# Kernel tuning notes

Hardware: AMD Instinct MI355X
Metric: run time of the kernel (lower is better)

Reference implementation:

```python
import jax, jax.numpy as jnp
import numpy as np

N_NODES = 50000


def sage_conv(x, src, dst, Wl, bl, Wr):
    # PyG SAGEConv (aggr='mean'): out_i = Wl @ mean_{j in N(i)} x_j + bl + Wr @ x_i
    msg = x[src]                                              # [E, d] gather
    agg = jax.ops.segment_sum(msg, dst, num_segments=N_NODES)  # [N, d]
    cnt = jax.ops.segment_sum(jnp.ones((src.shape[0],), x.dtype), dst,
                              num_segments=N_NODES)
    mean = agg / jnp.maximum(cnt, 1.0)[:, None]
    return mean @ Wl.T + bl + x @ Wr.T


def graph_forward(x, edge_index, W1l, b1, W1r, W2l, b2, W2r):
    src, dst = edge_index[0], edge_index[1]
    h = jnp.tanh(sage_conv(x, src, dst, W1l, b1, W1r))
    return jnp.tanh(sage_conv(h, src, dst, W2l, b2, W2r))


def setup_inputs() -> dict:
    key = jax.random.key(0)
    ks = jax.random.split(key, 16)
    E = 800000
    IN, HID, OUT = 128, 256, 128
    s = lambda fan: 1.0 / np.sqrt(fan)
    inp = {
        'x0': jax.random.normal(ks[0], (N_NODES, IN), jnp.float32),
        'x1': jax.random.normal(ks[1], (N_NODES, IN), jnp.float32),
        'edge_index0': jax.random.randint(ks[2], (2, E), 0, N_NODES),
        'edge_index1': jax.random.randint(ks[3], (2, E), 0, N_NODES),
    }
    for g, base in ((0, 4), (1, 10)):
        inp[f'W1l_{g}'] = jax.random.normal(ks[base + 0], (HID, IN), jnp.float32) * s(IN)
        inp[f'b1_{g}'] = jnp.zeros((HID,), jnp.float32)
        inp[f'W1r_{g}'] = jax.random.normal(ks[base + 1], (HID, IN), jnp.float32) * s(IN)
        inp[f'W2l_{g}'] = jax.random.normal(ks[base + 2], (OUT, HID), jnp.float32) * s(HID)
        inp[f'b2_{g}'] = jnp.zeros((OUT,), jnp.float32)
        inp[f'W2r_{g}'] = jax.random.normal(ks[base + 3], (OUT, HID), jnp.float32) * s(HID)
    return inp


def reference(x0, x1, edge_index0, edge_index1,
              W1l_0, b1_0, W1r_0, W2l_0, b2_0, W2r_0,
              W1l_1, b1_1, W1r_1, W2l_1, b2_1, W2r_1):
    out0 = graph_forward(x0, edge_index0, W1l_0, b1_0, W1r_0, W2l_0, b2_0, W2r_0)
    out1 = graph_forward(x1, edge_index1, W1l_1, b1_1, W1r_1, W2l_1, b2_1, W2r_1)
    return jnp.concatenate([out0, out1], axis=0)
```

## Files before the change

### kernel.cpp

```cpp
#include <hip/hip_runtime.h>
#include <cstddef>

#define N_NODES 50000
#define N_EDGES 800000
#define CAP 64
#define XU (N_NODES * 16)
#define XRNG ((N_NODES + 7) / 8)

typedef __attribute__((ext_vector_type(8))) _Float16 half8;
typedef __attribute__((ext_vector_type(2))) _Float16 half2v;
typedef __attribute__((ext_vector_type(4))) float f32x4;
typedef __attribute__((ext_vector_type(4))) float f4v;
typedef __attribute__((ext_vector_type(2))) float f2v;

__device__ __forceinline__ float fast_tanh(float x) {
    float t = __expf(2.0f * x);
    return 1.0f - 2.0f / (t + 1.0f);
}

__global__ __launch_bounds__(256) void prep_k(
        const int* __restrict__ src0, const int* __restrict__ dst0,
        const int* __restrict__ src1, const int* __restrict__ dst1,
        int* __restrict__ cnt, int* __restrict__ adj,
        const float* __restrict__ x0, const float* __restrict__ x1,
        const float* __restrict__ w00, const float* __restrict__ w01,
        const float* __restrict__ w02, const float* __restrict__ w03,
        const float* __restrict__ w10, const float* __restrict__ w11,
        const float* __restrict__ w12, const float* __restrict__ w13,
        _Float16* __restrict__ xd, _Float16* __restrict__ wd) {
    const int triple = blockIdx.x >> 3;
    const int role3 = triple % 3;
    const int grp = blockIdx.x & 7;
    if (role3 < 2) {
        const int ftriple = (triple / 3) * 2 + role3;
        const int g = grp >> 2;
        const int lo = (grp & 3) * (2 * XRNG), hi = lo + 2 * XRNG;
        const int* src = g ? src1 : src0;
        const int* dst = g ? dst1 : dst0;
        int* cg = cnt + g * N_NODES;
        int* ag = adj + (size_t)g * N_NODES * CAP;
        for (int e = ftriple * 256 + threadIdx.x; e < N_EDGES; e += 262144) {
            int d = __builtin_nontemporal_load(dst + e);
            if (d >= lo && d < hi) {
                int sv = __builtin_nontemporal_load(src + e);
                int c = atomicAdd(&cg[d], 1);
                if (c < CAP) ag[d * CAP + c] = sv;
            }
        }
    } else {
        const int slot = (triple / 3) * 8 + grp;
        const int total = 2 * XU + 32768;
        for (int i = slot * 256 + threadIdx.x; i < total; i += 4096 * 256) {
            const float* s; _Float16* d;
            if (i < 2 * XU) {
                int g = i >= XU ? 1 : 0;
                int l = i - g * XU;
                s = (g ? x1 : x0) + (size_t)l * 8;
                d = xd + (size_t)g * ((size_t)N_NODES * 256) + (size_t)l * 8;
            } else {
                int w = i - 2 * XU;
                int g = w >> 14, m = (w >> 12) & 3, l = w & 4095;
                const float* wm;
                if (g == 0) wm = (m == 0) ? w00 : (m == 1) ? w01 : (m == 2) ? w02 : w03;
                else        wm = (m == 0) ? w10 : (m == 1) ? w11 : (m == 2) ? w12 : w13;
                s = wm + (size_t)l * 8;
                d = wd + (size_t)g * 131072 + (size_t)m * 32768 + (size_t)l * 8;
            }
            f4v v0 = __builtin_nontemporal_load((const f4v*)s);
            f4v v1 = __builtin_nontemporal_load((const f4v*)s + 1);
            half8 o;
            o[0] = (_Float16)v0[0]; o[1] = (_Float16)v0[1];
            o[2] = (_Float16)v0[2]; o[3] = (_Float16)v0[3];
            o[4] = (_Float16)v1[0]; o[5] = (_Float16)v1[1];
            o[6] = (_Float16)v1[2]; o[7] = (_Float16)v1[3];
            __builtin_nontemporal_store(o, (half8*)d);
        }
    }
}

template <int OUTM, int RSU>
__global__ __launch_bounds__(256) void gather_mean_k(
        const unsigned* __restrict__ Xu, size_t xgs,
        const int* __restrict__ cnt, const int* __restrict__ adj,
        unsigned* __restrict__ outm, size_t ogs,
        const unsigned* __restrict__ Pu, size_t pgs,
        const float* __restrict__ bias0, const float* __restrict__ bias1,
        float* __restrict__ outf, int N) {
    const int g = blockIdx.y;
    int gw = blockIdx.x * 4 + (threadIdx.x >> 6);
    if (gw >= N) return;
    const int lane = threadIdx.x & 63;
    const int deg0 = cnt[g * N_NODES + gw];
    const int deg = deg0 < CAP ? deg0 : CAP;
    const int* aj = adj + (size_t)g * N_NODES * CAP + (size_t)gw * CAP;
    const unsigned* Xl = Xu + (size_t)g * xgs + lane;
    float sx = 0.f, sy = 0.f;
    int n = 0;
    for (; n + 16 <= deg; n += 16) {
        unsigned u0  = Xl[(size_t)aj[n     ] * RSU];
        unsigned u1  = Xl[(size_t)aj[n +  1] * RSU];
        unsigned u2  = Xl[(size_t)aj[n +  2] * RSU];
        unsigned u3  = Xl[(size_t)aj[n +  3] * RSU];
        unsigned u4  = Xl[(size_t)aj[n +  4] * RSU];
        unsigned u5  = Xl[(size_t)aj[n +  5] * RSU];
        unsigned u6  = Xl[(size_t)aj[n +  6] * RSU];
        unsigned u7  = Xl[(size_t)aj[n +  7] * RSU];
        unsigned u8  = Xl[(size_t)aj[n +  8] * RSU];
        unsigned u9  = Xl[(size_t)aj[n +  9] * RSU];
        unsigned u10 = Xl[(size_t)aj[n + 10] * RSU];
        unsigned u11 = Xl[(size_t)aj[n + 11] * RSU];
        unsigned u12 = Xl[(size_t)aj[n + 12] * RSU];
        unsigned u13 = Xl[(size_t)aj[n + 13] * RSU];
        unsigned u14 = Xl[(size_t)aj[n + 14] * RSU];
        unsigned u15 = Xl[(size_t)aj[n + 15] * RSU];
        half2v h0  = __builtin_bit_cast(half2v, u0);
        half2v h1  = __builtin_bit_cast(half2v, u1);
        half2v h2  = __builtin_bit_cast(half2v, u2);
        half2v h3  = __builtin_bit_cast(half2v, u3);
        half2v h4  = __builtin_bit_cast(half2v, u4);
        half2v h5  = __builtin_bit_cast(half2v, u5);
        half2v h6  = __builtin_bit_cast(half2v, u6);
        half2v h7  = __builtin_bit_cast(half2v, u7);
        half2v h8  = __builtin_bit_cast(half2v, u8);
        half2v h9  = __builtin_bit_cast(half2v, u9);
        half2v h10 = __builtin_bit_cast(half2v, u10);
        half2v h11 = __builtin_bit_cast(half2v, u11);
        half2v h12 = __builtin_bit_cast(half2v, u12);
        half2v h13 = __builtin_bit_cast(half2v, u13);
        half2v h14 = __builtin_bit_cast(half2v, u14);
        half2v h15 = __builtin_bit_cast(half2v, u15);
        sx += (float)h0.x + (float)h1.x + (float)h2.x + (float)h3.x
            + (float)h4.x + (float)h5.x + (float)h6.x + (float)h7.x
            + (float)h8.x + (float)h9.x + (float)h10.x + (float)h11.x
            + (float)h12.x + (float)h13.x + (float)h14.x + (float)h15.x;
        sy += (float)h0.y + (float)h1.y + (float)h2.y + (float)h3.y
            + (float)h4.y + (float)h5.y + (float)h6.y + (float)h7.y
            + (float)h8.y + (float)h9.y + (float)h10.y + (float)h11.y
            + (float)h12.y + (float)h13.y + (float)h14.y + (float)h15.y;
    }
    for (; n + 4 <= deg; n += 4) {
        unsigned u0 = Xl[(size_t)aj[n    ] * RSU];
        unsigned u1 = Xl[(size_t)aj[n + 1] * RSU];
        unsigned u2 = Xl[(size_t)aj[n + 2] * RSU];
        unsigned u3 = Xl[(size_t)aj[n + 3] * RSU];
        half2v h0 = __builtin_bit_cast(half2v, u0);
        half2v h1 = __builtin_bit_cast(half2v, u1);
        half2v h2 = __builtin_bit_cast(half2v, u2);
        half2v h3 = __builtin_bit_cast(half2v, u3);
        sx += (float)h0.x + (float)h1.x + (float)h2.x + (float)h3.x;
        sy += (float)h0.y + (float)h1.y + (float)h2.y + (float)h3.y;
    }
    for (; n < deg; n++) {
        unsigned u = Xl[(size_t)aj[n] * RSU];
        half2v h = __builtin_bit_cast(half2v, u);
        sx += (float)h.x;
        sy += (float)h.y;
    }
    float inv = 1.0f / (float)(deg0 > 0 ? deg0 : 1);
    float mx = sx * inv, my = sy * inv;
    if (OUTM == 0) {
        half2v o;
        o.x = (_Float16)mx; o.y = (_Float16)my;
        outm[(size_t)g * ogs + (size_t)gw * 64 + lane] =
            __builtin_bit_cast(unsigned, o);
    } else {
        unsigned pu = __builtin_nontemporal_load(
            Pu + (size_t)g * pgs + (size_t)gw * 64 + lane);
        half2v ph = __builtin_bit_cast(half2v, pu);
        const float* bias = g ? bias1 : bias0;
        float2 bb = ((const float2*)bias)[lane];
        f2v o;
        o.x = fast_tanh(mx + (float)ph.x + bb.x);
        o.y = fast_tanh(my + (float)ph.y + bb.y);
        __builtin_nontemporal_store(
            o, (f2v*)(outf + (size_t)g * N_NODES * 128) + (size_t)gw * 64 + lane);
    }
}

#define TM 128
#define TN 64
#define TK 32
#define LSTR 40
#define OSTR 72
#define SMEM_BYTES (TM * OSTR * 2)

template <bool TANH>
__global__ __launch_bounds__(256)
void gemm_f16_k(const _Float16* __restrict__ A1a, const _Float16* __restrict__ A1b,
                const _Float16* __restrict__ B1a, const _Float16* __restrict__ B1b,
                int K1,
                const _Float16* __restrict__ A2a, const _Float16* __restrict__ A2b,
                const _Float16* __restrict__ B2a, const _Float16* __restrict__ B2b,
                int K2,
                const float* __restrict__ biasa, const float* __restrict__ biasb,
                _Float16* __restrict__ outLoA, _Float16* __restrict__ outLoB,
                _Float16* __restrict__ outHiA, _Float16* __restrict__ outHiB,
                int MdLo, int MdHi, int N) {
    const int gz = blockIdx.z;
    const _Float16* A1 = gz ? A1b : A1a;
    const _Float16* B1 = gz ? B1b : B1a;
    const _Float16* A2 = gz ? A2b : A2a;
    const _Float16* B2 = gz ? B2b : B2a;
    const float* bias  = gz ? biasb : biasa;
    _Float16* outLo    = gz ? outLoB : outLoA;
    _Float16* outHi    = gz ? outHiB : outHiA;

    __shared__ char smem[SMEM_BYTES];
    _Float16 (*sA)[LSTR] = reinterpret_cast<_Float16(*)[LSTR]>(smem);
    _Float16 (*sB)[LSTR] = reinterpret_cast<_Float16(*)[LSTR]>(smem + TM * LSTR * 2);
    _Float16 (*sO)[OSTR] = reinterpret_cast<_Float16(*)[OSTR]>(smem);

    const int tid = threadIdx.x;
    const int lane = tid & 63;
    const int wave = tid >> 6;
    const int waveM = (wave & 1) * 64;
    const int waveN = (wave >> 1) * 32;
    const int rowBase = blockIdx.y * TM;
    const int colBase = blockIdx.x * TN;
    const int Ktot = K1 + K2;

    const int r0 = tid >> 2, c0 = tid & 3;
    const int r1 = r0 + 64;
    const int gr0 = rowBase + r0, gr1 = rowBase + r1;

    f32x4 acc[4][2] = {};
    half8 pA0, pA1, pB0;

    auto load_tile = [&](int k0) {
        const _Float16 *A, *B; int ko, ld;
        if (k0 < K1) { A = A1; B = B1; ko = k0;      ld = K1; }
        else         { A = A2; B = B2; ko = k0 - K1; ld = K2; }
        half8 z = {(_Float16)0, (_Float16)0, (_Float16)0, (_Float16)0,
                   (_Float16)0, (_Float16)0, (_Float16)0, (_Float16)0};
        size_t a0 = (size_t)gr0 * ld + ko + c0 * 8;
        size_t a1 = (size_t)gr1 * ld + ko + c0 * 8;
        pA0 = gr0 < N ? *(const half8*)(A + a0) : z;
        pA1 = gr1 < N ? *(const half8*)(A + a1) : z;
        pB0 = *(const half8*)(B + (size_t)(colBase + r0) * ld + ko + c0 * 8);
    };
    auto store_tile = [&]() {
        *(half8*)&sA[r0][c0 * 8] = pA0;
        *(half8*)&sA[r1][c0 * 8] = pA1;
        *(half8*)&sB[r0][c0 * 8] = pB0;
    };

    const int fm = lane & 15;
    const int fq = (lane >> 4) * 8;
    half8 fa[4], fb[2];
    auto read_frags = [&]() {
        #pragma unroll
        for (int mi = 0; mi < 4; mi++)
            fa[mi] = *(const half8*)&sA[waveM + mi * 16 + fm][fq];
        #pragma unroll
        for (int ni = 0; ni < 2; ni++)
            fb[ni] = *(const half8*)&sB[waveN + ni * 16 + fm][fq];
    };
    auto mfma_all = [&]() {
        #pragma unroll
        for (int mi = 0; mi < 4; mi++)
            #pragma unroll
            for (int ni = 0; ni < 2; ni++)
                acc[mi][ni] = __builtin_amdgcn_mfma_f32_16x16x32_f16(
                    fa[mi], fb[ni], acc[mi][ni], 0, 0, 0);
    };

    load_tile(0);
    store_tile();
    __syncthreads();

    for (int k0 = TK; k0 < Ktot; k0 += TK) {
        read_frags();
        load_tile(k0);
        mfma_all();
        __syncthreads();
        store_tile();
        __syncthreads();
    }
    read_frags();
    mfma_all();

    __syncthreads();
    {
        const int lr0 = waveM + (lane >> 4) * 4;
        const int lc0 = waveN + fm;
        #pragma unroll
        for (int ni = 0; ni < 2; ni++) {
            float bv = bias ? bias[colBase + lc0 + ni * 16] : 0.0f;
            #pragma unroll
            for (int mi = 0; mi < 4; mi++)
                #pragma unroll
                for (int r = 0; r < 4; r++) {
                    float v = acc[mi][ni][r] + bv;
                    if (TANH) v = fast_tanh(v);
                    sO[lr0 + mi * 16 + r][lc0 + ni * 16] = (_Float16)v;
                }
        }
    }
    __syncthreads();
    {
        _Float16* outp; int Md, cb;
        if (colBase < 128) { outp = outLo; Md = MdLo; cb = colBase; }
        else               { outp = outHi; Md = MdHi; cb = colBase - 128; }
        const int rr = tid >> 3;
        const int cc = (tid & 7) * 8;
        #pragma unroll
        for (int p = 0; p < 4; p++) {
            int row = p * 32 + rr;
            int grow = rowBase + row;
            if (grow < N)
                *(half8*)(outp + (size_t)grow * Md + cb + cc) =
                    *(const half8*)&sO[row][cc];
        }
    }
}

extern "C" void kernel_launch(void* const* d_in, const int* in_sizes, int n_in,
                              void* d_out, int out_size, void* d_ws, size_t ws_size,
                              hipStream_t stream) {
    const int N = N_NODES, E = N_EDGES;

    const float* x[2]   = {(const float*)d_in[0],  (const float*)d_in[1]};
    const int*   ei[2]  = {(const int*)d_in[2],    (const int*)d_in[3]};
    const float* W1l[2] = {(const float*)d_in[4],  (const float*)d_in[10]};
    const float* b1[2]  = {(const float*)d_in[5],  (const float*)d_in[11]};
    const float* W1r[2] = {(const float*)d_in[6],  (const float*)d_in[12]};
    const float* W2l[2] = {(const float*)d_in[7],  (const float*)d_in[13]};
    const float* b2[2]  = {(const float*)d_in[8],  (const float*)d_in[14]};
    const float* W2r[2] = {(const float*)d_in[9],  (const float*)d_in[15]};
    float* out = (float*)d_out;

    char* wsb = (char*)d_ws;
    const size_t MiB = 1u << 20;
    int*      cnt  = (int*)(wsb);
    int*      adj  = (int*)(wsb + 1 * MiB);
    _Float16* Wh   = (_Float16*)(wsb + 27 * MiB);
    _Float16* feat = (_Float16*)(wsb + 28 * MiB);
    _Float16* h16  = (_Float16*)(wsb + 80 * MiB);

    const size_t FGS  = (size_t)N * 256;
    const size_t WGS  = 131072;
    const size_t HSTR = (size_t)N * 256;

    const int gemm_rows = (N + TM - 1) / TM;
    const int agg_x = N / 4;

    (void)hipMemsetAsync(cnt, 0, 2 * (size_t)N * sizeof(int), stream);
    prep_k<<<12288, 256, 0, stream>>>(
        ei[0], ei[0] + E, ei[1], ei[1] + E, cnt, adj,
        x[0], x[1],
        W1l[0], W1r[0], W2l[0], W2r[0],
        W1l[1], W1r[1], W2l[1], W2r[1],
        feat, Wh);

    gather_mean_k<0, 64><<<dim3(agg_x, 2), 256, 0, stream>>>(
        (const unsigned*)feat, FGS / 2, cnt, adj,
        (unsigned*)(feat + (size_t)N * 128), FGS / 2,
        nullptr, 0, nullptr, nullptr, nullptr, N);

    _Float16* x16g[2]   = {feat, feat + FGS};
    _Float16* mean16[2] = {feat + (size_t)N * 128, feat + FGS + (size_t)N * 128};
    _Float16* z16[2]    = {feat, feat + FGS};
    _Float16* po16[2]   = {mean16[0], mean16[1]};
    _Float16* W1l16[2]  = {Wh, Wh + WGS};
    _Float16* W1r16[2]  = {Wh + 32768, Wh + WGS + 32768};
    _Float16* W2cat[2]  = {Wh + 65536, Wh + WGS + 65536};

    if (ws_size >= (size_t)132 * MiB) {
        _Float16* h0 = h16;
        _Float16* h1 = h16 + HSTR;
        gemm_f16_k<true><<<dim3(4, gemm_rows, 2), 256, 0, stream>>>(
            mean16[0], mean16[1], W1l16[0], W1l16[1], 128,
            x16g[0], x16g[1], W1r16[0], W1r16[1], 128,
            b1[0], b1[1], h0, h1, h0 + 128, h1 + 128, 256, 256, N);
        gemm_f16_k<false><<<dim3(4, gemm_rows, 2), 256, 0, stream>>>(
            h0, h1, W2cat[0], W2cat[1], 256,
            nullptr, nullptr, nullptr, nullptr, 0,
            nullptr, nullptr, z16[0], z16[1], po16[0], po16[1], 128, 128, N);
    } else {
        for (int g = 0; g < 2; g++) {
            gemm_f16_k<true><<<dim3(4, gemm_rows, 1), 256, 0, stream>>>(
                mean16[g], mean16[g], W1l16[g], W1l16[g], 128,
                x16g[g], x16g[g], W1r16[g], W1r16[g], 128,
                b1[g], b1[g], h16, h16, h16 + 128, h16 + 128, 256, 256, N);
            gemm_f16_k<false><<<dim3(4, gemm_rows, 1), 256, 0, stream>>>(
                h16, h16, W2cat[g], W2cat[g], 256,
                nullptr, nullptr, nullptr, nullptr, 0,
                nullptr, nullptr, z16[g], z16[g], po16[g], po16[g], 128, 128, N);
        }
    }

    gather_mean_k<1, 64><<<dim3(agg_x, 2), 256, 0, stream>>>(
        (const unsigned*)feat, FGS / 2, cnt, adj,
        nullptr, 0,
        (const unsigned*)(feat + (size_t)N * 128), FGS / 2,
        b2[0], b2[1], out, N);
}
```

Measured before the change: 393.8 us.

## Interleave GEMM and gather blocks across graphs in mixed persistent kernels

Restructures the schedule so the two independent graphs are staggered. A new mix_k kernel interleaves GEMM tiles of one graph with gather blocks of the other in a 1:8 ratio, so the compute-bound MFMA work overlaps the latency-bound irregular gathers. The aim is to hide gather memory latency and fill idle compute units. In exchange it adds branching and shared-memory reservation in gather blocks, which may lower occupancy, and the first and last gathers still run alone.

```diff
diff --git a/kernel.cpp b/kernel.cpp
--- a/kernel.cpp
+++ b/kernel.cpp
@@ -184,28 +184,12 @@
 #define OSTR 72
 #define SMEM_BYTES (TM * OSTR * 2)
 
-template <bool TANH>
-__global__ __launch_bounds__(256)
-void gemm_f16_k(const _Float16* __restrict__ A1a, const _Float16* __restrict__ A1b,
-                const _Float16* __restrict__ B1a, const _Float16* __restrict__ B1b,
-                int K1,
-                const _Float16* __restrict__ A2a, const _Float16* __restrict__ A2b,
-                const _Float16* __restrict__ B2a, const _Float16* __restrict__ B2b,
-                int K2,
-                const float* __restrict__ biasa, const float* __restrict__ biasb,
-                _Float16* __restrict__ outLoA, _Float16* __restrict__ outLoB,
-                _Float16* __restrict__ outHiA, _Float16* __restrict__ outHiB,
-                int MdLo, int MdHi, int N) {
-    const int gz = blockIdx.z;
-    const _Float16* A1 = gz ? A1b : A1a;
-    const _Float16* B1 = gz ? B1b : B1a;
-    const _Float16* A2 = gz ? A2b : A2a;
-    const _Float16* B2 = gz ? B2b : B2a;
-    const float* bias  = gz ? biasb : biasa;
-    _Float16* outLo    = gz ? outLoB : outLoA;
-    _Float16* outHi    = gz ? outHiB : outHiA;
-
-    __shared__ char smem[SMEM_BYTES];
+__device__ __forceinline__ void gemm_core(
+        const _Float16* __restrict__ A1, const _Float16* __restrict__ B1, int K1,
+        const _Float16* __restrict__ A2, const _Float16* __restrict__ B2, int K2,
+        const float* __restrict__ bias, int tanhf,
+        _Float16* __restrict__ outLo, _Float16* __restrict__ outHi,
+        int MdLo, int MdHi, int bx, int by, int N, char* smem) {
     _Float16 (*sA)[LSTR] = reinterpret_cast<_Float16(*)[LSTR]>(smem);
     _Float16 (*sB)[LSTR] = reinterpret_cast<_Float16(*)[LSTR]>(smem + TM * LSTR * 2);
     _Float16 (*sO)[OSTR] = reinterpret_cast<_Float16(*)[OSTR]>(smem);
@@ -215,8 +199,8 @@
     const int wave = tid >> 6;
     const int waveM = (wave & 1) * 64;
     const int waveN = (wave >> 1) * 32;
-    const int rowBase = blockIdx.y * TM;
-    const int colBase = blockIdx.x * TN;
+    const int rowBase = by * TM;
+    const int colBase = bx * TN;
     const int Ktot = K1 + K2;
 
     const int r0 = tid >> 2, c0 = tid & 3;
@@ -291,7 +275,7 @@
                 #pragma unroll
                 for (int r = 0; r < 4; r++) {
                     float v = acc[mi][ni][r] + bv;
-                    if (TANH) v = fast_tanh(v);
+                    if (tanhf) v = fast_tanh(v);
                     sO[lr0 + mi * 16 + r][lc0 + ni * 16] = (_Float16)v;
                 }
         }
@@ -314,6 +298,158 @@
     }
 }
 
+__device__ __forceinline__ void gather_core(
+        const unsigned* __restrict__ Xu, const int* __restrict__ cnt,
+        const int* __restrict__ adj, unsigned* __restrict__ outm,
+        const unsigned* __restrict__ Pu, const float* __restrict__ bias,
+        float* __restrict__ outf, int mode, int b, int N) {
+    int gw = b * 4 + (threadIdx.x >> 6);
+    if (gw >= N) return;
+    const int lane = threadIdx.x & 63;
+    const int deg0 = cnt[gw];
+    const int deg = deg0 < CAP ? deg0 : CAP;
+    const int* aj = adj + (size_t)gw * CAP;
+    const unsigned* Xl = Xu + lane;
+    float sx = 0.f, sy = 0.f;
+    int n = 0;
+    for (; n + 16 <= deg; n += 16) {
+        unsigned u0  = Xl[(size_t)aj[n     ] * 64];
+        unsigned u1  = Xl[(size_t)aj[n +  1] * 64];
+        unsigned u2  = Xl[(size_t)aj[n +  2] * 64];
+        unsigned u3  = Xl[(size_t)aj[n +  3] * 64];
+        unsigned u4  = Xl[(size_t)aj[n +  4] * 64];
+        unsigned u5  = Xl[(size_t)aj[n +  5] * 64];
+        unsigned u6  = Xl[(size_t)aj[n +  6] * 64];
+        unsigned u7  = Xl[(size_t)aj[n +  7] * 64];
+        unsigned u8  = Xl[(size_t)aj[n +  8] * 64];
+        unsigned u9  = Xl[(size_t)aj[n +  9] * 64];
+        unsigned u10 = Xl[(size_t)aj[n + 10] * 64];
+        unsigned u11 = Xl[(size_t)aj[n + 11] * 64];
+        unsigned u12 = Xl[(size_t)aj[n + 12] * 64];
+        unsigned u13 = Xl[(size_t)aj[n + 13] * 64];
+        unsigned u14 = Xl[(size_t)aj[n + 14] * 64];
+        unsigned u15 = Xl[(size_t)aj[n + 15] * 64];
+        half2v h0  = __builtin_bit_cast(half2v, u0);
+        half2v h1  = __builtin_bit_cast(half2v, u1);
+        half2v h2  = __builtin_bit_cast(half2v, u2);
+        half2v h3  = __builtin_bit_cast(half2v, u3);
+        half2v h4  = __builtin_bit_cast(half2v, u4);
+        half2v h5  = __builtin_bit_cast(half2v, u5);
+        half2v h6  = __builtin_bit_cast(half2v, u6);
+        half2v h7  = __builtin_bit_cast(half2v, u7);
+        half2v h8  = __builtin_bit_cast(half2v, u8);
+        half2v h9  = __builtin_bit_cast(half2v, u9);
+        half2v h10 = __builtin_bit_cast(half2v, u10);
+        half2v h11 = __builtin_bit_cast(half2v, u11);
+        half2v h12 = __builtin_bit_cast(half2v, u12);
+        half2v h13 = __builtin_bit_cast(half2v, u13);
+        half2v h14 = __builtin_bit_cast(half2v, u14);
+        half2v h15 = __builtin_bit_cast(half2v, u15);
+        sx += (float)h0.x + (float)h1.x + (float)h2.x + (float)h3.x
+            + (float)h4.x + (float)h5.x + (float)h6.x + (float)h7.x
+            + (float)h8.x + (float)h9.x + (float)h10.x + (float)h11.x
+            + (float)h12.x + (float)h13.x + (float)h14.x + (float)h15.x;
+        sy += (float)h0.y + (float)h1.y + (float)h2.y + (float)h3.y
+            + (float)h4.y + (float)h5.y + (float)h6.y + (float)h7.y
+            + (float)h8.y + (float)h9.y + (float)h10.y + (float)h11.y
+            + (float)h12.y + (float)h13.y + (float)h14.y + (float)h15.y;
+    }
+    for (; n + 4 <= deg; n += 4) {
+        unsigned u0 = Xl[(size_t)aj[n    ] * 64];
+        unsigned u1 = Xl[(size_t)aj[n + 1] * 64];
+        unsigned u2 = Xl[(size_t)aj[n + 2] * 64];
+        unsigned u3 = Xl[(size_t)aj[n + 3] * 64];
+        half2v h0 = __builtin_bit_cast(half2v, u0);
+        half2v h1 = __builtin_bit_cast(half2v, u1);
+        half2v h2 = __builtin_bit_cast(half2v, u2);
+        half2v h3 = __builtin_bit_cast(half2v, u3);
+        sx += (float)h0.x + (float)h1.x + (float)h2.x + (float)h3.x;
+        sy += (float)h0.y + (float)h1.y + (float)h2.y + (float)h3.y;
+    }
+    for (; n < deg; n++) {
+        unsigned u = Xl[(size_t)aj[n] * 64];
+        half2v h = __builtin_bit_cast(half2v, u);
+        sx += (float)h.x;
+        sy += (float)h.y;
+    }
+    float inv = 1.0f / (float)(deg0 > 0 ? deg0 : 1);
+    float mx = sx * inv, my = sy * inv;
+    if (mode == 0) {
+        half2v o;
+        o.x = (_Float16)mx; o.y = (_Float16)my;
+        outm[(size_t)gw * 64 + lane] = __builtin_bit_cast(unsigned, o);
+    } else {
+        unsigned pu = __builtin_nontemporal_load(Pu + (size_t)gw * 64 + lane);
+        half2v ph = __builtin_bit_cast(half2v, pu);
+        float2 bb = ((const float2*)bias)[lane];
+        f2v o;
+        o.x = fast_tanh(mx + (float)ph.x + bb.x);
+        o.y = fast_tanh(my + (float)ph.y + bb.y);
+        __builtin_nontemporal_store(o, (f2v*)outf + (size_t)gw * 64 + lane);
+    }
+}
+
+__global__ __launch_bounds__(256) void mix_k(
+        const _Float16* A1a, const _Float16* B1a, int K1a,
+        const _Float16* A2a, const _Float16* B2a, int K2a,
+        const float* biasa, int tanha,
+        _Float16* outLoA, _Float16* outHiA, int MdLoA, int MdHiA,
+        const _Float16* A1b, const _Float16* B1b, int K1b,
+        const _Float16* A2b, const _Float16* B2b, int K2b,
+        const float* biasb, int tanhb,
+        _Float16* outLoB, _Float16* outHiB, int MdLoB, int MdHiB,
+        int nGemmJobs, int gemmRows,
+        const unsigned* Xu, const int* cnt, const int* adj,
+        unsigned* outm, const unsigned* Pu, const float* gbias,
+        float* outf, int gmode, int nGatherBlocks, int N) {
+    __shared__ char smem[SMEM_BYTES];
+    const int perJob = 4 * gemmRows;
+    const int nG = nGemmJobs * perJob;
+    int gemmIdx = -1, gatherIdx = -1;
+    if (nGatherBlocks == 0) {
+        gemmIdx = blockIdx.x;
+    } else if (nG == 0) {
+        gatherIdx = blockIdx.x;
+    } else {
+        int q = blockIdx.x / 9, r = blockIdx.x % 9;
+        if (r == 8) gemmIdx = q;
+        else        gatherIdx = q * 8 + r;
+    }
+    if (gemmIdx >= 0 && gemmIdx < nG) {
+        const int jb = gemmIdx >= perJob;
+        const int r = jb ? gemmIdx - perJob : gemmIdx;
+        gemm_core(jb ? A1b : A1a, jb ? B1b : B1a, jb ? K1b : K1a,
+                  jb ? A2b : A2a, jb ? B2b : B2a, jb ? K2b : K2a,
+                  jb ? biasb : biasa, jb ? tanhb : tanha,
+                  jb ? outLoB : outLoA, jb ? outHiB : outHiA,
+                  jb ? MdLoB : MdLoA, jb ? MdHiB : MdHiA,
+                  r % 4, r / 4, N, smem);
+    } else if (gatherIdx >= 0 && gatherIdx < nGatherBlocks) {
+        gather_core(Xu, cnt, adj, outm, Pu, gbias, outf, gmode, gatherIdx, N);
+    }
+}
+
+template <bool TANH>
+__global__ __launch_bounds__(256)
+void gemm_f16_k(const _Float16* __restrict__ A1a, const _Float16* __restrict__ A1b,
+                const _Float16* __restrict__ B1a, const _Float16* __restrict__ B1b,
+                int K1,
+                const _Float16* __restrict__ A2a, const _Float16* __restrict__ A2b,
+                const _Float16* __restrict__ B2a, const _Float16* __restrict__ B2b,
+                int K2,
+                const float* __restrict__ biasa, const float* __restrict__ biasb,
+                _Float16* __restrict__ outLoA, _Float16* __restrict__ outLoB,
+                _Float16* __restrict__ outHiA, _Float16* __restrict__ outHiB,
+                int MdLo, int MdHi, int N) {
+    __shared__ char smem[SMEM_BYTES];
+    const int gz = blockIdx.z;
+    gemm_core(gz ? A1b : A1a, gz ? B1b : B1a, K1,
+              gz ? A2b : A2a, gz ? B2b : B2a, K2,
+              gz ? biasb : biasa, TANH ? 1 : 0,
+              gz ? outLoB : outLoA, gz ? outHiB : outHiA,
+              MdLo, MdHi, blockIdx.x, blockIdx.y, N, smem);
+}
+
 extern "C" void kernel_launch(void* const* d_in, const int* in_sizes, int n_in,
                               void* d_out, int out_size, void* d_ws, size_t ws_size,
                               hipStream_t stream) {
@@ -342,6 +478,7 @@
     const size_t HSTR = (size_t)N * 256;
 
     const int gemm_rows = (N + TM - 1) / TM;
+    const int perJob = 4 * gemm_rows;
     const int agg_x = N / 4;
 
     (void)hipMemsetAsync(cnt, 0, 2 * (size_t)N * sizeof(int), stream);
@@ -352,11 +489,6 @@
         W1l[1], W1r[1], W2l[1], W2r[1],
         feat, Wh);
 
-    gather_mean_k<0, 64><<<dim3(agg_x, 2), 256, 0, stream>>>(
-        (const unsigned*)feat, FGS / 2, cnt, adj,
-        (unsigned*)(feat + (size_t)N * 128), FGS / 2,
-        nullptr, 0, nullptr, nullptr, nullptr, N);
-
     _Float16* x16g[2]   = {feat, feat + FGS};
     _Float16* mean16[2] = {feat + (size_t)N * 128, feat + FGS + (size_t)N * 128};
     _Float16* z16[2]    = {feat, feat + FGS};
@@ -364,19 +496,49 @@
     _Float16* W1l16[2]  = {Wh, Wh + WGS};
     _Float16* W1r16[2]  = {Wh + 32768, Wh + WGS + 32768};
     _Float16* W2cat[2]  = {Wh + 65536, Wh + WGS + 65536};
+    int*      cntg[2]   = {cnt, cnt + N};
+    int*      adjg[2]   = {adj, adj + (size_t)N * CAP};
 
     if (ws_size >= (size_t)132 * MiB) {
         _Float16* h0 = h16;
         _Float16* h1 = h16 + HSTR;
-        gemm_f16_k<true><<<dim3(4, gemm_rows, 2), 256, 0, stream>>>(
-            mean16[0], mean16[1], W1l16[0], W1l16[1], 128,
-            x16g[0], x16g[1], W1r16[0], W1r16[1], 128,
-            b1[0], b1[1], h0, h1, h0 + 128, h1 + 128, 256, 256, N);
-        gemm_f16_k<false><<<dim3(4, gemm_rows, 2), 256, 0, stream>>>(
-            h0, h1, W2cat[0], W2cat[1], 256,
-            nullptr, nullptr, nullptr, nullptr, 0,
-            nullptr, nullptr, z16[0], z16[1], po16[0], po16[1], 128, 128, N);
+        const int mixed = perJob * 9;
+        gather_mean_k<0, 64><<<dim3(agg_x, 1), 256, 0, stream>>>(
+            (const unsigned*)x16g[0], 0, cntg[0], adjg[0],
+            (unsigned*)mean16[0], 0, nullptr, 0, nullptr, nullptr, nullptr, N);
+        mix_k<<<mixed, 256, 0, stream>>>(
+            mean16[0], W1l16[0], 128, x16g[0], W1r16[0], 128, b1[0], 1,
+            h0, h0 + 128, 256, 256,
+            mean16[0], W1l16[0], 128, x16g[0], W1r16[0], 128, b1[0], 1,
+            h0, h0 + 128, 256, 256,
+            1, gemm_rows,
+            (const unsigned*)x16g[1], cntg[1], adjg[1],
+            (unsigned*)mean16[1], nullptr, nullptr, nullptr, 0, agg_x, N);
+        mix_k<<<2 * perJob, 256, 0, stream>>>(
+            h0, W2cat[0], 256, nullptr, nullptr, 0, nullptr, 0,
+            z16[0], po16[0], 128, 128,
+            mean16[1], W1l16[1], 128, x16g[1], W1r16[1], 128, b1[1], 1,
+            h1, h1 + 128, 256, 256,
+            2, gemm_rows,
+            nullptr, nullptr, nullptr, nullptr, nullptr, nullptr,
+            nullptr, 0, 0, N);
+        mix_k<<<mixed, 256, 0, stream>>>(
+            h1, W2cat[1], 256, nullptr, nullptr, 0, nullptr, 0,
+            z16[1], po16[1], 128, 128,
+            h1, W2cat[1], 256, nullptr, nullptr, 0, nullptr, 0,
+            z16[1], po16[1], 128, 128,
+            1, gemm_rows,
+            (const unsigned*)z16[0], cntg[0], adjg[0],
+            nullptr, (const unsigned*)po16[0], b2[0], out, 1, agg_x, N);
+        gather_mean_k<1, 64><<<dim3(agg_x, 1), 256, 0, stream>>>(
+            (const unsigned*)z16[1], 0, cntg[1], adjg[1],
+            nullptr, 0, (const unsigned*)po16[1], 0,
+            b2[1], nullptr, out + (size_t)N * 128, N);
     } else {
+        gather_mean_k<0, 64><<<dim3(agg_x, 2), 256, 0, stream>>>(
+            (const unsigned*)feat, FGS / 2, cnt, adj,
+            (unsigned*)(feat + (size_t)N * 128), FGS / 2,
+            nullptr, 0, nullptr, nullptr, nullptr, N);
         for (int g = 0; g < 2; g++) {
             gemm_f16_k<true><<<dim3(4, gemm_rows, 1), 256, 0, stream>>>(
                 mean16[g], mean16[g], W1l16[g], W1l16[g], 128,
@@ -387,11 +549,10 @@
                 nullptr, nullptr, nullptr, nullptr, 0,
                 nullptr, nullptr, z16[g], z16[g], po16[g], po16[g], 128, 128, N);
         }
-    }
-
-    gather_mean_k<1, 64><<<dim3(agg_x, 2), 256, 0, stream>>>(
-        (const unsigned*)feat, FGS / 2, cnt, adj,
-        nullptr, 0,
-        (const unsigned*)(feat + (size_t)N * 128), FGS / 2,
-        b2[0], b2[1], out, N);
-}
+        gather_mean_k<1, 64><<<dim3(agg_x, 2), 256, 0, stream>>>(
+            (const unsigned*)feat, FGS / 2, cnt, adj,
+            nullptr, 0,
+            (const unsigned*)(feat + (size_t)N * 128), FGS / 2,
+            b2[0], b2[1], out, N);
+    }
+}
```

Result: slower. 417.9 us (+6.1%).
